# Performance work log

Measured on AMD Instinct MI355X. Metric: run time of the kernel, lower is better.

Reference implementation:

```python
import jax, jax.numpy as jnp
import numpy as np

N_NODES = 4096
N_EDGES = 524288
IN_DIM = 6
EMB_N = 4
EMB_D = 8
EDGE_D = 1
HID = 64
N_HEADS = 4
LN_EPS = 1e-5


def _layernorm(h, g, b):
    m = jnp.mean(h, axis=-1, keepdims=True)
    v = jnp.mean(jnp.square(h - m), axis=-1, keepdims=True)
    return (h - m) * jax.lax.rsqrt(v + LN_EPS) * g + b


def setup_inputs() -> dict:
    key = jax.random.key(0)
    ks = jax.random.split(key, 16)
    s = lambda fan_in: 1.0 / np.sqrt(fan_in)
    inp = {
        'x': jax.random.normal(ks[0], (N_NODES, IN_DIM), jnp.float32),
        'edge_attr': jax.random.uniform(ks[1], (N_EDGES, EDGE_D), jnp.float32),
        'entity_emb': jax.random.normal(ks[2], (EMB_N, EMB_D), jnp.float32),
        'lin1_w': jax.random.uniform(ks[3], (HID, IN_DIM + EMB_D + EDGE_D), jnp.float32, -s(15), s(15)),
        'lin1_b': jnp.zeros((HID,), jnp.float32),
        'lay_w': jax.random.uniform(ks[4], (HID, HID), jnp.float32, -s(HID), s(HID)),
        'lay_b': jnp.zeros((HID,), jnp.float32),
        'ln_g': jnp.ones((HID,), jnp.float32),
        'ln_b': jnp.zeros((HID,), jnp.float32),
        'in_proj_w': jax.random.uniform(ks[5], (3 * HID, HID), jnp.float32, -s(HID), s(HID)),
        'in_proj_b': jnp.zeros((3 * HID,), jnp.float32),
        'out_proj_w': jax.random.uniform(ks[6], (HID, HID), jnp.float32, -s(HID), s(HID)),
        'out_proj_b': jnp.zeros((HID,), jnp.float32),
        'an_g': jnp.ones((HID,), jnp.float32),
        'an_b': jnp.zeros((HID,), jnp.float32),
        'out_w': jax.random.uniform(ks[7], (HID, HID), jnp.float32, -s(HID), s(HID)),
        'out_b': jnp.zeros((HID,), jnp.float32),
        'edge_index': jax.random.randint(ks[8], (2, N_EDGES), 0, N_NODES, jnp.int64),
        'entity_type': jax.random.randint(ks[9], (N_NODES,), 0, EMB_N, jnp.int64),
    }
    return inp


def reference(x, edge_attr, entity_emb, lin1_w, lin1_b, lay_w, lay_b, ln_g, ln_b,
              in_proj_w, in_proj_b, out_proj_w, out_proj_b, an_g, an_b, out_w, out_b,
              edge_index, entity_type):
    # --- EmbedConv ---
    # concat node features with entity embedding: [N, 6+8]
    xe = jnp.concatenate([x, entity_emb[entity_type]], axis=-1)
    src, dst = edge_index[0], edge_index[1]
    # gather source nodes + edge attr: [E, 15]
    msg = jnp.concatenate([xe[src], edge_attr], axis=-1)
    msg = _layernorm(jax.nn.relu(msg @ lin1_w.T + lin1_b), ln_g, ln_b)
    # layer_N = 1 extra layer, shared LayerNorm
    msg = _layernorm(jax.nn.relu(msg @ lay_w.T + lay_b), ln_g, ln_b)
    # scatter-add aggregate into destination nodes: [N, 64]
    h = jax.ops.segment_sum(msg, dst, num_segments=N_NODES)
    # --- MultiheadAttention over all nodes as one sequence (eval: no dropout) ---
    qkv = h @ in_proj_w.T + in_proj_b  # [N, 3H]
    q, k, v = jnp.split(qkv, 3, axis=-1)
    hd = HID // N_HEADS
    q = q.reshape(N_NODES, N_HEADS, hd).transpose(1, 0, 2)  # [h, n, d]
    k = k.reshape(N_NODES, N_HEADS, hd).transpose(1, 0, 2)
    v = v.reshape(N_NODES, N_HEADS, hd).transpose(1, 0, 2)
    scores = jnp.einsum('hnd,hmd->hnm', q, k) / np.sqrt(hd)
    attn = jax.nn.softmax(scores, axis=-1)
    o = jnp.einsum('hnm,hmd->hnd', attn, v).transpose(1, 0, 2).reshape(N_NODES, HID)
    o = o @ out_proj_w.T + out_proj_b
    h = _layernorm(h + o, an_g, an_b)
    # --- output layer ---
    return h @ out_w.T + out_b
```

## Files before the change

kernel.cpp:

```cpp
#include <hip/hip_runtime.h>

#define N_NODES 4096
#define N_EDGES 524288
#define HID 64

typedef short short8 __attribute__((ext_vector_type(8)));
typedef float f32x4 __attribute__((ext_vector_type(4)));
typedef float f32x16 __attribute__((ext_vector_type(16)));

__device__ __forceinline__ float bcastf(float v, int l) {
    return __int_as_float(__builtin_amdgcn_readlane(__float_as_int(v), l));
}

__device__ __forceinline__ void wave_sum2(float& a, float& b) {
    #pragma unroll
    for (int off = 32; off > 0; off >>= 1) {
        a += __shfl_xor(a, off, 64);
        b += __shfl_xor(b, off, 64);
    }
}

__device__ __forceinline__ short f2bf(float f) {
    unsigned u = __float_as_uint(f);
    u = u + 0x7FFFu + ((u >> 16) & 1u);
    return (short)(u >> 16);
}
__device__ __forceinline__ float bf2f(short s) {
    return __uint_as_float(((unsigned)(unsigned short)s) << 16);
}
__device__ __forceinline__ void split_cheap(float f, short& hi, short& lo) {
    unsigned u = __float_as_uint(f);
    unsigned hb = u & 0xffff0000u;
    float lof = f - __uint_as_float(hb);
    hi = (short)(u >> 16);
    lo = (short)(__float_as_uint(lof) >> 16);
}

__device__ __forceinline__ void pack_plane8(const float* vv, short8& ah, short8& al) {
    union { unsigned u[4]; short8 s; } Uh, Ul;
    #pragma unroll
    for (int i = 0; i < 4; i++) {
        unsigned hw;
        asm("v_cvt_pk_bf16_f32 %0, %1, %2" : "=v"(hw) : "v"(vv[2 * i]), "v"(vv[2 * i + 1]));
        float he = __uint_as_float(hw << 16);
        float ho = __uint_as_float(hw & 0xffff0000u);
        float le = vv[2 * i] - he;
        float lo_ = vv[2 * i + 1] - ho;
        unsigned lw;
        asm("v_cvt_pk_bf16_f32 %0, %1, %2" : "=v"(lw) : "v"(le), "v"(lo_));
        Uh.u[i] = hw; Ul.u[i] = lw;
    }
    ah = Uh.s; al = Ul.s;
}

__global__ void hist_prep(const float* __restrict__ x, const float* __restrict__ emb,
                          const int* __restrict__ etype, const int* __restrict__ ei,
                          const float* __restrict__ w1, const float* __restrict__ b1,
                          const float* __restrict__ w2, const float* __restrict__ lng,
                          const float* __restrict__ lnb, const float* __restrict__ b2,
                          const float* __restrict__ ipw,
                          float* __restrict__ A1, int* __restrict__ cnt, int* __restrict__ rank,
                          unsigned short* __restrict__ w2fh, unsigned short* __restrict__ w2fl,
                          unsigned short* __restrict__ ipfh, unsigned short* __restrict__ ipfl,
                          float* __restrict__ b2p, float* __restrict__ w14p) {
    int tid = blockIdx.x * 256 + threadIdx.x;
    int d = ei[N_EDGES + tid];
    rank[tid] = atomicAdd(&cnt[d], 1);
    if (tid < N_NODES * 64) {
        int n = tid >> 6, f = tid & 63;
        const float* wr = w1 + f * 15;
        float acc = b1[f];
        #pragma unroll
        for (int k = 0; k < 6; k++) acc = fmaf(x[n * 6 + k], wr[k], acc);
        int e = etype[n];
        #pragma unroll
        for (int k = 0; k < 8; k++) acc = fmaf(emb[e * 8 + k], wr[6 + k], acc);
        A1[tid] = acc;
    }
    if (tid < 4096) {
        int idx = tid >> 9, ln = (tid >> 3) & 63, j = tid & 7;
        int mm = ln & 15, qq = ln >> 4;
        int g = idx >> 1, tt = idx & 1;
        int col = tt * 32 + qq * 8 + j;
        float w = w2[(g * 16 + mm) * 64 + col] * lng[col];
        short hi = f2bf(w);
        w2fh[tid] = (unsigned short)hi;
        w2fl[tid] = (unsigned short)f2bf(w - bf2f(hi));
    }
    if (tid < 12288) {
        int idx = tid >> 9, ln = (tid >> 3) & 63, j = tid & 7;
        int mm = ln & 15, qq = ln >> 4;
        int og = idx >> 1, tt = idx & 1;
        float w = ipw[(og * 16 + mm) * 64 + tt * 32 + qq * 8 + j];
        short hi = f2bf(w);
        ipfh[tid] = (unsigned short)hi;
        ipfl[tid] = (unsigned short)f2bf(w - bf2f(hi));
    }
    if (tid < 64) {
        float acc = b2[tid];
        for (int c = 0; c < 64; c++) acc = fmaf(w2[tid * 64 + c], lnb[c], acc);
        b2p[tid] = acc;
        w14p[tid] = w1[tid * 15 + 14];
    }
}

__global__ void __launch_bounds__(256) scatter_scan(
        const int* __restrict__ cnt, const int* __restrict__ ei,
        const float* __restrict__ edge_attr, const int* __restrict__ rank,
        int* __restrict__ bnd,
        int* __restrict__ ssrc, float* __restrict__ sea) {
    __shared__ int lbnd[4096];
    __shared__ int wsum[4];
    int t = threadIdx.x;
    int base = t * 16;
    int v16[16];
    int T = 0;
    #pragma unroll
    for (int j4 = 0; j4 < 4; j4++) {
        int4 c4 = ((const int4*)cnt)[t * 4 + j4];
        v16[j4 * 4 + 0] = c4.x; v16[j4 * 4 + 1] = c4.y;
        v16[j4 * 4 + 2] = c4.z; v16[j4 * 4 + 3] = c4.w;
        T += c4.x + c4.y + c4.z + c4.w;
    }
    int inc = T;
    int l = t & 63;
    #pragma unroll
    for (int off = 1; off < 64; off <<= 1) {
        int v = __shfl_up(inc, off, 64);
        if (l >= off) inc += v;
    }
    if (l == 63) wsum[t >> 6] = inc;
    __syncthreads();
    int wo = 0;
    for (int w = 0; w < (t >> 6); w++) wo += wsum[w];
    int run = wo + inc - T;
    #pragma unroll
    for (int j = 0; j < 16; j++) {
        lbnd[base + j] = run;
        run += v16[j];
    }
    if (blockIdx.x == 0) {
        #pragma unroll
        for (int j = 0; j < 16; j++) bnd[base + j] = lbnd[base + j];
        if (t == 255) bnd[4096] = run;
    }
    __syncthreads();
    int e = blockIdx.x * 256 + t;
    int d = ei[N_EDGES + e];
    int pos = lbnd[d] + rank[e];
    ssrc[pos] = ei[e];
    sea[pos] = edge_attr[e];
}

__global__ void __launch_bounds__(256, 3) edge_gather_mfma(
        const float* __restrict__ A1,
        const int* __restrict__ ssrc, const float* __restrict__ sea,
        const int* __restrict__ bnd,
        const unsigned short* __restrict__ w2fh, const unsigned short* __restrict__ w2fl,
        const float* __restrict__ w14p, const float* __restrict__ b2p,
        const float* __restrict__ lg, const float* __restrict__ lb,
        float* __restrict__ h) {
    __shared__ uint4 lw2h4[512];
    __shared__ uint4 lw2l4[512];
    int tid = threadIdx.x;
    {
        const uint4* gh = (const uint4*)w2fh;
        const uint4* gl = (const uint4*)w2fl;
        lw2h4[tid] = gh[tid];
        lw2h4[tid + 256] = gh[tid + 256];
        lw2l4[tid] = gl[tid];
        lw2l4[tid + 256] = gl[tid + 256];
    }
    const unsigned short* lw2h = (const unsigned short*)lw2h4;
    const unsigned short* lw2l = (const unsigned short*)lw2l4;

    int lane = tid & 63;
    int wv = tid >> 6;
    int m = lane & 15;
    int q = lane >> 4;

    float w14f[16];
    {
        float4 wa = *(const float4*)(w14p + q * 8);
        float4 wb = *(const float4*)(w14p + q * 8 + 4);
        float4 wc = *(const float4*)(w14p + 32 + q * 8);
        float4 wd = *(const float4*)(w14p + 32 + q * 8 + 4);
        w14f[0] = wa.x; w14f[1] = wa.y; w14f[2] = wa.z; w14f[3] = wa.w;
        w14f[4] = wb.x; w14f[5] = wb.y; w14f[6] = wb.z; w14f[7] = wb.w;
        w14f[8] = wc.x; w14f[9] = wc.y; w14f[10] = wc.z; w14f[11] = wc.w;
        w14f[12] = wd.x; w14f[13] = wd.y; w14f[14] = wd.z; w14f[15] = wd.w;
    }
    float b2v[16];
    #pragma unroll
    for (int g = 0; g < 4; g++) {
        float4 bb = *(const float4*)(b2p + g * 16 + q * 4);
        b2v[g * 4 + 0] = bb.x; b2v[g * 4 + 1] = bb.y;
        b2v[g * 4 + 2] = bb.z; b2v[g * 4 + 3] = bb.w;
    }
    __syncthreads();

    for (int node = blockIdx.x * 4 + wv; node < N_NODES; node += 3072) {
        int start = bnd[node], end = bnd[node + 1];
        int ntiles = (end - start + 15) >> 4;
        float acc[16];
        #pragma unroll
        for (int i = 0; i < 16; i++) acc[i] = 0.f;

        int srcn = 0; float eav = 0.f;
        float4 va = {0,0,0,0}, vb = {0,0,0,0}, vc = {0,0,0,0}, vd = {0,0,0,0};
        if (ntiles > 0) {
            int ec = start + m; if (ec >= end) ec = end - 1;
            srcn = ssrc[ec]; eav = sea[ec];
            const float* ar = A1 + srcn * 64 + q * 8;
            va = *(const float4*)(ar);
            vb = *(const float4*)(ar + 4);
            vc = *(const float4*)(ar + 32);
            vd = *(const float4*)(ar + 36);
        }
        for (int t = 0; t < ntiles; t++) {
            int base = start + t * 16;
            float v[16] = {va.x, va.y, va.z, va.w, vb.x, vb.y, vb.z, vb.w,
                           vc.x, vc.y, vc.z, vc.w, vd.x, vd.y, vd.z, vd.w};
            float eavc = eav;
            if (t + 1 < ntiles) {
                int e2 = base + 16 + m; if (e2 >= end) e2 = end - 1;
                int srcn2 = ssrc[e2]; eav = sea[e2];
                const float* ar2 = A1 + srcn2 * 64 + q * 8;
                va = *(const float4*)(ar2);
                vb = *(const float4*)(ar2 + 4);
                vc = *(const float4*)(ar2 + 32);
                vd = *(const float4*)(ar2 + 36);
            }
            float s = 0.f, s2 = 0.f;
            #pragma unroll
            for (int j = 0; j < 16; j++) {
                float u = fmaxf(fmaf(w14f[j], eavc, v[j]), 0.f);
                v[j] = u;
                s += u;
                s2 = fmaf(u, u, s2);
            }
            s += __shfl_xor(s, 16, 64);  s2 += __shfl_xor(s2, 16, 64);
            s += __shfl_xor(s, 32, 64);  s2 += __shfl_xor(s2, 32, 64);
            float mean = s * (1.f / 64.f);
            float var = s2 * (1.f / 64.f) - mean * mean;
            float rs = rsqrtf(var + 1e-5f);
            float a0 = -mean * rs;
            #pragma unroll
            for (int j = 0; j < 16; j++) v[j] = fmaf(v[j], rs, a0);
            short8 a2h[2], a2l[2];
            pack_plane8(v, a2h[0], a2l[0]);
            pack_plane8(v + 8, a2h[1], a2l[1]);
            int ob = (t >> 20);
            float s_ = 0.f, s2_ = 0.f;
            float t2v[16];
            #pragma unroll
            for (int g = 0; g < 4; g++) {
                f32x4 c = {0.f, 0.f, 0.f, 0.f};
                #pragma unroll
                for (int t2 = 0; t2 < 2; t2++) {
                    short8 bh = *(const short8*)(lw2h + ((g * 2 + t2) * 64 + lane + ob) * 8);
                    short8 bl = *(const short8*)(lw2l + ((g * 2 + t2) * 64 + lane + ob) * 8);
                    c = __builtin_amdgcn_mfma_f32_16x16x32_bf16(bh, a2l[t2], c, 0, 0, 0);
                    c = __builtin_amdgcn_mfma_f32_16x16x32_bf16(bl, a2h[t2], c, 0, 0, 0);
                    c = __builtin_amdgcn_mfma_f32_16x16x32_bf16(bh, a2h[t2], c, 0, 0, 0);
                }
                #pragma unroll
                for (int r = 0; r < 4; r++) {
                    float vv = fmaxf(c[r] + b2v[g * 4 + r], 0.f);
                    t2v[g * 4 + r] = vv;
                    s_ += vv;
                    s2_ = fmaf(vv, vv, s2_);
                }
            }
            s_ += __shfl_xor(s_, 16, 64);  s2_ += __shfl_xor(s2_, 16, 64);
            s_ += __shfl_xor(s_, 32, 64);  s2_ += __shfl_xor(s2_, 32, 64);
            float mean2 = s_ * (1.f / 64.f);
            float var2 = s2_ * (1.f / 64.f) - mean2 * mean2;
            float rs2 = rsqrtf(var2 + 1e-5f);
            float a02 = -mean2 * rs2;
            if (base + m < end) {
                #pragma unroll
                for (int i = 0; i < 16; i++) acc[i] += fmaf(t2v[i], rs2, a02);
            }
        }
        #pragma unroll
        for (int off = 1; off < 16; off <<= 1)
            #pragma unroll
            for (int i = 0; i < 16; i++) acc[i] += __shfl_xor(acc[i], off, 64);
        if (m == 0) {
            float deg = (float)(end - start);
            #pragma unroll
            for (int g = 0; g < 4; g++) {
                float4 lgv = *(const float4*)(lg + g * 16 + q * 4);
                float4 lbv = *(const float4*)(lb + g * 16 + q * 4);
                float* hp = h + node * 64 + g * 16 + q * 4;
                hp[0] = lgv.x * acc[g * 4 + 0] + deg * lbv.x;
                hp[1] = lgv.y * acc[g * 4 + 1] + deg * lbv.y;
                hp[2] = lgv.z * acc[g * 4 + 2] + deg * lbv.z;
                hp[3] = lgv.w * acc[g * 4 + 3] + deg * lbv.w;
            }
        }
    }
}

__global__ void __launch_bounds__(256) qkv_mfma(
        const float* __restrict__ h, const float* __restrict__ b,
        const unsigned short* __restrict__ ipfh, const unsigned short* __restrict__ ipfl,
        unsigned short* __restrict__ qhp, unsigned short* __restrict__ qlp,
        unsigned short* __restrict__ khp, unsigned short* __restrict__ klp,
        unsigned short* __restrict__ vT) {
    int lane = threadIdx.x & 63;
    int wv = threadIdx.x >> 6;
    int m = lane & 15;
    int q = lane >> 4;
    int wid = blockIdx.x * 4 + wv;
    int tile = wid / 12;
    int og = wid - tile * 12;
    short8 bh[2], bl[2];
    #pragma unroll
    for (int t = 0; t < 2; t++) {
        bh[t] = *(const short8*)(ipfh + ((og * 2 + t) * 64 + lane) * 8);
        bl[t] = *(const short8*)(ipfl + ((og * 2 + t) * 64 + lane) * 8);
    }
    f32x4 c = {0.f, 0.f, 0.f, 0.f};
    #pragma unroll
    for (int t = 0; t < 2; t++) {
        const float* hr = h + (tile * 16 + m) * 64 + t * 32 + q * 8;
        float4 f0 = *(const float4*)hr;
        float4 f1 = *(const float4*)(hr + 4);
        float av8[8] = {f0.x, f0.y, f0.z, f0.w, f1.x, f1.y, f1.z, f1.w};
        short8 ah, al;
        #pragma unroll
        for (int j = 0; j < 8; j++) {
            short hi, lo;
            split_cheap(av8[j], hi, lo);
            ah[j] = hi;
            al[j] = lo;
        }
        c = __builtin_amdgcn_mfma_f32_16x16x32_bf16(al, bh[t], c, 0, 0, 0);
        c = __builtin_amdgcn_mfma_f32_16x16x32_bf16(ah, bl[t], c, 0, 0, 0);
        c = __builtin_amdgcn_mfma_f32_16x16x32_bf16(ah, bh[t], c, 0, 0, 0);
    }
    int o = og * 16 + m;
    float bias = b[o];
    #pragma unroll
    for (int r = 0; r < 4; r++) {
        int node = tile * 16 + q * 4 + r;
        float val = c[r] + bias;
        if (og < 4) {
            float aq = val * (0.25f * 1.44269504f);
            size_t idx = ((size_t)(og * N_NODES + node)) * 16 + m;
            short hi = f2bf(aq);
            qhp[idx] = (unsigned short)hi;
            qlp[idx] = (unsigned short)f2bf(aq - bf2f(hi));
        } else if (og < 8) {
            size_t idx = ((size_t)((og - 4) * N_NODES + node)) * 16 + m;
            short hi = f2bf(val);
            khp[idx] = (unsigned short)hi;
            klp[idx] = (unsigned short)f2bf(val - bf2f(hi));
        } else {
            int feat = (og - 8) * 16 + m;
            vT[(size_t)feat * N_NODES + node] = (unsigned short)f2bf(val);
        }
    }
}

__global__ void __launch_bounds__(256) attn_mfma(
        const unsigned short* __restrict__ qhp, const unsigned short* __restrict__ qlp,
        const unsigned short* __restrict__ khp, const unsigned short* __restrict__ klp,
        const unsigned short* __restrict__ vT,
        float* __restrict__ part_o, float* __restrict__ part_ml) {
    int lane = threadIdx.x & 63;
    int wv = threadIdx.x >> 6;
    int l31 = lane & 31;
    int hi = lane >> 5;
    const short8 vones = {0x3F80, 0x3F80, 0x3F80, 0x3F80, 0x3F80, 0x3F80, 0x3F80, 0x3F80};

    int wid = blockIdx.x * 4 + wv;
    int kc = wid & 7;
    int wqt = (wid >> 3) & 127;
    int head = wid >> 10;

    int qrow = wqt * 32 + l31;
    short8 aqh = *(const short8*)(qhp + ((size_t)(head * N_NODES + qrow)) * 16 + hi * 8);
    short8 aql = *(const short8*)(qlp + ((size_t)(head * N_NODES + qrow)) * 16 + hi * 8);

    const unsigned short* khb = khp + (size_t)head * N_NODES * 16;
    const unsigned short* klb = klp + (size_t)head * N_NODES * 16;
    const unsigned short* vtb = vT + (size_t)(head * 16 + (l31 & 15)) * N_NODES;

    float mS = -3e38f;
    f32x16 Ot = {0.f, 0.f, 0.f, 0.f, 0.f, 0.f, 0.f, 0.f,
                 0.f, 0.f, 0.f, 0.f, 0.f, 0.f, 0.f, 0.f};

    size_t koff = ((size_t)(kc * 512 + l31)) * 16 + hi * 8;
    short8 bkh = *(const short8*)(khb + koff);
    short8 bkl = *(const short8*)(klb + koff);

    for (int bb = 0; bb < 16; bb++) {
        int n0 = kc * 512 + bb * 32;
        int nbb = (bb + 1 < 16) ? (bb + 1) : 15;
        size_t koffn = ((size_t)(kc * 512 + nbb * 32 + l31)) * 16 + hi * 8;
        short8 nkh = *(const short8*)(khb + koffn);
        short8 nkl = *(const short8*)(klb + koffn);
        f32x16 S = {0.f, 0.f, 0.f, 0.f, 0.f, 0.f, 0.f, 0.f,
                    0.f, 0.f, 0.f, 0.f, 0.f, 0.f, 0.f, 0.f};
        S = __builtin_amdgcn_mfma_f32_32x32x16_bf16(bkh, aql, S, 0, 0, 0);
        S = __builtin_amdgcn_mfma_f32_32x32x16_bf16(bkl, aqh, S, 0, 0, 0);
        S = __builtin_amdgcn_mfma_f32_32x32x16_bf16(bkh, aqh, S, 0, 0, 0);
        float mr = S[0];
        #pragma unroll
        for (int r = 1; r < 16; r++) mr = fmaxf(mr, S[r]);
        mr = fmaxf(mr, __shfl_xor(mr, 32, 64));
        if (!__all(mr <= mS)) {
            float mn = fmaxf(mS, mr);
            float alpha = exp2f(mS - mn);
            mS = mn;
            #pragma unroll
            for (int r = 0; r < 9; r++) Ot[r] *= alpha;
        }
        float p[16];
        #pragma unroll
        for (int r = 0; r < 16; r++) p[r] = exp2f(S[r] - mS);
        unsigned w0, w1, w2, w3, u0, u1, u2, u3;
        asm("v_cvt_pk_bf16_f32 %0, %1, %2" : "=v"(w0) : "v"(p[0]), "v"(p[1]));
        asm("v_cvt_pk_bf16_f32 %0, %1, %2" : "=v"(w1) : "v"(p[2]), "v"(p[3]));
        asm("v_cvt_pk_bf16_f32 %0, %1, %2" : "=v"(w2) : "v"(p[4]), "v"(p[5]));
        asm("v_cvt_pk_bf16_f32 %0, %1, %2" : "=v"(w3) : "v"(p[6]), "v"(p[7]));
        asm("v_cvt_pk_bf16_f32 %0, %1, %2" : "=v"(u0) : "v"(p[8]), "v"(p[9]));
        asm("v_cvt_pk_bf16_f32 %0, %1, %2" : "=v"(u1) : "v"(p[10]), "v"(p[11]));
        asm("v_cvt_pk_bf16_f32 %0, %1, %2" : "=v"(u2) : "v"(p[12]), "v"(p[13]));
        asm("v_cvt_pk_bf16_f32 %0, %1, %2" : "=v"(u3) : "v"(p[14]), "v"(p[15]));
        asm("v_permlane32_swap_b32 %0, %1" : "+v"(w0), "+v"(w2));
        asm("v_permlane32_swap_b32 %0, %1" : "+v"(w1), "+v"(w3));
        asm("v_permlane32_swap_b32 %0, %1" : "+v"(u0), "+v"(u2));
        asm("v_permlane32_swap_b32 %0, %1" : "+v"(u1), "+v"(u3));
        union { unsigned u[4]; short8 s; } pf0, pf1;
        pf0.u[0] = w0; pf0.u[1] = w1; pf0.u[2] = w2; pf0.u[3] = w3;
        pf1.u[0] = u0; pf1.u[1] = u1; pf1.u[2] = u2; pf1.u[3] = u3;
        short8 v0, v1;
        if (l31 < 16) {
            v0 = *(const short8*)(vtb + n0 + hi * 8);
            v1 = *(const short8*)(vtb + n0 + 16 + hi * 8);
        } else if (l31 == 16) {
            v0 = vones; v1 = vones;
        } else {
            v0 = (short8)0; v1 = (short8)0;
        }
        Ot = __builtin_amdgcn_mfma_f32_32x32x16_bf16(v0, pf0.s, Ot, 0, 0, 0);
        Ot = __builtin_amdgcn_mfma_f32_32x32x16_bf16(v1, pf1.s, Ot, 0, 0, 0);
        bkh = nkh; bkl = nkl;
    }
    int qt16 = wqt * 2 + (l31 >> 4);
    int qi = l31 & 15;
    size_t pb = ((size_t)(head * 8 + kc) * 256 + qt16) * 256;
    f32x4 o0 = {Ot[0], Ot[1], Ot[2], Ot[3]};
    f32x4 o1 = {Ot[4], Ot[5], Ot[6], Ot[7]};
    *(f32x4*)(part_o + pb + qi * 16 + hi * 4) = o0;
    *(f32x4*)(part_o + pb + qi * 16 + 8 + hi * 4) = o1;
    if (lane < 32) {
        size_t mb = ((size_t)(head * 8 + kc) * 256 + qt16) * 32;
        part_ml[mb + qi] = mS;
        part_ml[mb + 16 + qi] = Ot[8];
    }
}

__global__ void post_kernel(const float* __restrict__ h,
                            const float* __restrict__ part_o, const float* __restrict__ part_ml,
                            const float* __restrict__ opw, const float* __restrict__ opb,
                            const float* __restrict__ ag, const float* __restrict__ ab,
                            const float* __restrict__ ow, const float* __restrict__ ob,
                            float* __restrict__ out) {
    __shared__ float wl1[64 * 65];
    __shared__ float wl2[64 * 65];
    for (int i = threadIdx.x; i < 4096; i += blockDim.x) {
        int r = i >> 6, c = i & 63;
        wl1[r * 65 + c] = opw[i];
        wl2[r * 65 + c] = ow[i];
    }
    __syncthreads();
    int lane = threadIdx.x & 63;
    int n = blockIdx.x * 4 + (threadIdx.x >> 6);
    int j = lane;
    int head = j >> 4, d = j & 15;
    int qt = n >> 4, qi = n & 15;
    float M = -3e38f, L = 0.f, Ov = 0.f;
    #pragma unroll
    for (int c = 0; c < 8; c++) {
        size_t base = ((size_t)(head * 8 + c) * 256 + qt);
        float mc = part_ml[base * 32 + qi];
        float lc = part_ml[base * 32 + 16 + qi];
        float ov = part_o[base * 256 + qi * 16 + d];
        if (mc > M) {
            float sc = exp2f(M - mc);
            M = mc;
            L = L * sc + lc;
            Ov = Ov * sc + ov;
        } else {
            float sc = exp2f(mc - M);
            L = fmaf(lc, sc, L);
            Ov = fmaf(ov, sc, Ov);
        }
    }
    float oj = Ov / L;
    float acc = opb[j];
    #pragma unroll
    for (int k = 0; k < 64; k++) acc = fmaf(wl1[j * 65 + k], bcastf(oj, k), acc);
    float r = h[n * 64 + j] + acc;
    float s = r, s2 = r * r;
    wave_sum2(s, s2);
    float mean = s * (1.f / 64.f);
    float var = s2 * (1.f / 64.f) - mean * mean;
    float hn = (r - mean) * rsqrtf(var + 1e-5f) * ag[j] + ab[j];
    float acc2 = ob[j];
    #pragma unroll
    for (int k = 0; k < 64; k++) acc2 = fmaf(wl2[j * 65 + k], bcastf(hn, k), acc2);
    out[n * 64 + j] = acc2;
}

extern "C" void kernel_launch(void* const* d_in, const int* in_sizes, int n_in,
                              void* d_out, int out_size, void* d_ws, size_t ws_size,
                              hipStream_t stream) {
    const float* x        = (const float*)d_in[0];
    const float* edge_attr= (const float*)d_in[1];
    const float* emb      = (const float*)d_in[2];
    const float* lin1_w   = (const float*)d_in[3];
    const float* lin1_b   = (const float*)d_in[4];
    const float* lay_w    = (const float*)d_in[5];
    const float* lay_b    = (const float*)d_in[6];
    const float* ln_g     = (const float*)d_in[7];
    const float* ln_b     = (const float*)d_in[8];
    const float* ipw      = (const float*)d_in[9];
    const float* ipb      = (const float*)d_in[10];
    const float* opw      = (const float*)d_in[11];
    const float* opb      = (const float*)d_in[12];
    const float* ang      = (const float*)d_in[13];
    const float* anb      = (const float*)d_in[14];
    const float* ow       = (const float*)d_in[15];
    const float* ob       = (const float*)d_in[16];
    const int*   ei       = (const int*)d_in[17];
    const int*   et       = (const int*)d_in[18];

    char* wsb = (char*)d_ws;
    size_t off = 0;
    float* A1             = (float*)(wsb + off);          off += 1048576;
    float* h              = (float*)(wsb + off);          off += 1048576;
    unsigned short* qhp   = (unsigned short*)(wsb + off); off += 524288;
    unsigned short* qlp   = (unsigned short*)(wsb + off); off += 524288;
    unsigned short* khp   = (unsigned short*)(wsb + off); off += 524288;
    unsigned short* klp   = (unsigned short*)(wsb + off); off += 524288;
    unsigned short* vT    = (unsigned short*)(wsb + off); off += 524288;
    float* part_o         = (float*)(wsb + off);          off += 8388608;
    float* part_ml        = (float*)(wsb + off);          off += 1048576;
    int*   cnt            = (int*)(wsb + off);            off += 16384;
    int*   bnd            = (int*)(wsb + off);            off += 16388;
    off = (off + 255) & ~(size_t)255;
    int*   rank           = (int*)(wsb + off);            off += 2097152;
    int*   ssrc           = (int*)(wsb + off);            off += 2097152;
    float* sea            = (float*)(wsb + off);          off += 2097152;
    unsigned short* w2fh  = (unsigned short*)(wsb + off); off += 8192;
    unsigned short* w2fl  = (unsigned short*)(wsb + off); off += 8192;
    unsigned short* ipfh  = (unsigned short*)(wsb + off); off += 24576;
    unsigned short* ipfl  = (unsigned short*)(wsb + off); off += 24576;
    float* b2p            = (float*)(wsb + off);          off += 256;
    float* w14p           = (float*)(wsb + off);          off += 256;

    (void)hipMemsetAsync(cnt, 0, 4096 * sizeof(int), stream);
    hist_prep<<<2048, 256, 0, stream>>>(x, emb, et, ei, lin1_w, lin1_b, lay_w, ln_g, ln_b,
                                        lay_b, ipw, A1, cnt, rank, w2fh, w2fl, ipfh, ipfl,
                                        b2p, w14p);
    scatter_scan<<<2048, 256, 0, stream>>>(cnt, ei, edge_attr, rank, bnd, ssrc, sea);
    edge_gather_mfma<<<768, 256, 0, stream>>>(A1, ssrc, sea, bnd, w2fh, w2fl,
                                              w14p, b2p, ln_g, ln_b, h);
    qkv_mfma<<<768, 256, 0, stream>>>(h, ipb, ipfh, ipfl, qhp, qlp, khp, klp, vT);
    attn_mfma<<<1024, 256, 0, stream>>>(qhp, qlp, khp, klp, vT, part_o, part_ml);
    post_kernel<<<1024, 256, 0, stream>>>(h, part_o, part_ml, opw, opb, ang, anb, ow, ob,
                                          (float*)d_out);
}
```

Baseline: 221.7 us.

## Fuse histogram and scatter-scan into one cooperative kernel with grid sync

Merges the histogram/weight-prep kernel and the scan/scatter kernel into a single cooperative launch of 1024 blocks, each handling two edges per thread and separated by a grid-wide barrier. Edge ranks, sources and attributes stay in registers across the barrier instead of going through a global rank array, which removes a kernel launch and a round trip of the rank buffer. In exchange it depends on cooperative launch residency (1024 blocks at 4 per CU) and pays the cost of a grid sync.

After: 340.0 us. +53.3%, slower.

```diff
diff --git a/kernel.cpp b/kernel.cpp
--- a/kernel.cpp
+++ b/kernel.cpp
@@ -1,4 +1,7 @@
 #include <hip/hip_runtime.h>
+#include <hip/hip_cooperative_groups.h>
+
+namespace cg = cooperative_groups;
 
 #define N_NODES 4096
 #define N_EDGES 524288
@@ -53,20 +56,34 @@
     ah = Uh.s; al = Ul.s;
 }
 
-__global__ void hist_prep(const float* __restrict__ x, const float* __restrict__ emb,
-                          const int* __restrict__ etype, const int* __restrict__ ei,
-                          const float* __restrict__ w1, const float* __restrict__ b1,
-                          const float* __restrict__ w2, const float* __restrict__ lng,
-                          const float* __restrict__ lnb, const float* __restrict__ b2,
-                          const float* __restrict__ ipw,
-                          float* __restrict__ A1, int* __restrict__ cnt, int* __restrict__ rank,
-                          unsigned short* __restrict__ w2fh, unsigned short* __restrict__ w2fl,
-                          unsigned short* __restrict__ ipfh, unsigned short* __restrict__ ipfl,
-                          float* __restrict__ b2p, float* __restrict__ w14p) {
-    int tid = blockIdx.x * 256 + threadIdx.x;
-    int d = ei[N_EDGES + tid];
-    rank[tid] = atomicAdd(&cnt[d], 1);
-    if (tid < N_NODES * 64) {
+__global__ void __launch_bounds__(256, 4) fused_pre(
+        const float* __restrict__ x, const float* __restrict__ emb,
+        const int* __restrict__ etype, const int* __restrict__ ei,
+        const float* __restrict__ edge_attr,
+        const float* __restrict__ w1, const float* __restrict__ b1,
+        const float* __restrict__ w2, const float* __restrict__ lng,
+        const float* __restrict__ lnb, const float* __restrict__ b2,
+        const float* __restrict__ ipw,
+        float* __restrict__ A1, int* __restrict__ cnt, int* __restrict__ bnd,
+        int* __restrict__ ssrc, float* __restrict__ sea,
+        unsigned short* __restrict__ w2fh, unsigned short* __restrict__ w2fl,
+        unsigned short* __restrict__ ipfh, unsigned short* __restrict__ ipfl,
+        float* __restrict__ b2p, float* __restrict__ w14p) {
+    __shared__ int lbnd[4096];
+    __shared__ int wsum[4];
+    int t = threadIdx.x;
+    int tid = blockIdx.x * 256 + t;
+    int e0 = blockIdx.x * 512 + t;
+    int e1 = e0 + 256;
+    int d0 = ei[N_EDGES + e0];
+    int d1 = ei[N_EDGES + e1];
+    int s0 = ei[e0];
+    int s1 = ei[e1];
+    float ea0 = edge_attr[e0];
+    float ea1 = edge_attr[e1];
+    int r0 = atomicAdd(&cnt[d0], 1);
+    int r1 = atomicAdd(&cnt[d1], 1);
+    {
         int n = tid >> 6, f = tid & 63;
         const float* wr = w1 + f * 15;
         float acc = b1[f];
@@ -102,16 +119,7 @@
         b2p[tid] = acc;
         w14p[tid] = w1[tid * 15 + 14];
     }
-}
-
-__global__ void __launch_bounds__(256) scatter_scan(
-        const int* __restrict__ cnt, const int* __restrict__ ei,
-        const float* __restrict__ edge_attr, const int* __restrict__ rank,
-        int* __restrict__ bnd,
-        int* __restrict__ ssrc, float* __restrict__ sea) {
-    __shared__ int lbnd[4096];
-    __shared__ int wsum[4];
-    int t = threadIdx.x;
+    cg::this_grid().sync();
     int base = t * 16;
     int v16[16];
     int T = 0;
@@ -145,11 +153,10 @@
         if (t == 255) bnd[4096] = run;
     }
     __syncthreads();
-    int e = blockIdx.x * 256 + t;
-    int d = ei[N_EDGES + e];
-    int pos = lbnd[d] + rank[e];
-    ssrc[pos] = ei[e];
-    sea[pos] = edge_attr[e];
+    int pos0 = lbnd[d0] + r0;
+    ssrc[pos0] = s0; sea[pos0] = ea0;
+    int pos1 = lbnd[d1] + r1;
+    ssrc[pos1] = s1; sea[pos1] = ea1;
 }
 
 __global__ void __launch_bounds__(256, 3) edge_gather_mfma(
@@ -555,7 +562,6 @@
     int*   cnt            = (int*)(wsb + off);            off += 16384;
     int*   bnd            = (int*)(wsb + off);            off += 16388;
     off = (off + 255) & ~(size_t)255;
-    int*   rank           = (int*)(wsb + off);            off += 2097152;
     int*   ssrc           = (int*)(wsb + off);            off += 2097152;
     float* sea            = (float*)(wsb + off);          off += 2097152;
     unsigned short* w2fh  = (unsigned short*)(wsb + off); off += 8192;
@@ -566,10 +572,19 @@
     float* w14p           = (float*)(wsb + off);          off += 256;
 
     (void)hipMemsetAsync(cnt, 0, 4096 * sizeof(int), stream);
-    hist_prep<<<2048, 256, 0, stream>>>(x, emb, et, ei, lin1_w, lin1_b, lay_w, ln_g, ln_b,
-                                        lay_b, ipw, A1, cnt, rank, w2fh, w2fl, ipfh, ipfl,
-                                        b2p, w14p);
-    scatter_scan<<<2048, 256, 0, stream>>>(cnt, ei, edge_attr, rank, bnd, ssrc, sea);
+    {
+        void* kargs[] = {
+            (void*)&x, (void*)&emb, (void*)&et, (void*)&ei, (void*)&edge_attr,
+            (void*)&lin1_w, (void*)&lin1_b, (void*)&lay_w, (void*)&ln_g,
+            (void*)&ln_b, (void*)&lay_b, (void*)&ipw,
+            (void*)&A1, (void*)&cnt, (void*)&bnd,
+            (void*)&ssrc, (void*)&sea,
+            (void*)&w2fh, (void*)&w2fl, (void*)&ipfh, (void*)&ipfl,
+            (void*)&b2p, (void*)&w14p
+        };
+        (void)hipLaunchCooperativeKernel((const void*)fused_pre, dim3(1024), dim3(256),
+                                         kargs, 0, stream);
+    }
     edge_gather_mfma<<<768, 256, 0, stream>>>(A1, ssrc, sea, bnd, w2fh, w2fl,
                                               w14p, b2p, ln_g, ln_b, h);
     qkv_mfma<<<768, 256, 0, stream>>>(h, ipb, ipfh, ipfl, qhp, qlp, khp, klp, vT);
```
